# Kernel tuning notes

Hardware: AMD Instinct MI355X
Metric: run time of the kernel (lower is better)

## Reference

```python
import jax, jax.numpy as jnp
import numpy as np
import math

T, C = 8192, 1024

def setup_inputs() -> dict:
    key = jax.random.key(0)
    ks = jax.random.split(key, 10)
    s = 1.0 / math.sqrt(C)
    return {
        "x": jax.random.normal(ks[0], (T, C), dtype=jnp.float32),
        "Wq": jax.random.normal(ks[1], (C, C), dtype=jnp.float32) * s,
        "bq": jax.random.normal(ks[2], (C,), dtype=jnp.float32) * s,
        "Wk": jax.random.normal(ks[3], (C, C), dtype=jnp.float32) * s,
        "bk": jax.random.normal(ks[4], (C,), dtype=jnp.float32) * s,
        "Wv": jax.random.normal(ks[5], (C, C), dtype=jnp.float32) * s,
        "bv": jax.random.normal(ks[6], (C,), dtype=jnp.float32) * s,
        "Wp": jax.random.normal(ks[7], (C, C), dtype=jnp.float32) * s,
        "bp": jax.random.normal(ks[8], (C,), dtype=jnp.float32) * s,
    }

def reference(x, Wq, bq, Wk, bk, Wv, bv, Wp, bp):
    # Single-head causal self-attention over an unbatched (T, C) sequence.
    t, c = x.shape
    q = x @ Wq.T + bq          # (T, C)
    k = x @ Wk.T + bk          # (T, C)
    v = x @ Wv.T + bv          # (T, C)
    att = (q @ k.T) / math.sqrt(c)                      # (T, T)
    causal = jnp.tril(jnp.ones((t, t), dtype=bool))
    att = jnp.where(causal, att, -jnp.inf)
    att = jax.nn.softmax(att, axis=-1)
    y = att @ v                                         # (T, C)
    y = y @ Wp.T + bp
    return y
```

## Files before the change

### kernel.cpp

```cpp
#include <hip/hip_runtime.h>
#include <hip/hip_bf16.h>

typedef __bf16 bf16x8 __attribute__((ext_vector_type(8)));
typedef float f32x4 __attribute__((ext_vector_type(4)));

static constexpr int Tn = 8192;
static constexpr int Cn = 1024;

#define DEVI __device__ __forceinline__

DEVI float bf2f(ushort u) { union { uint i; float f; } c; c.i = ((uint)u) << 16; return c.f; }
DEVI ushort f2bf(float f) {
  uint x = __builtin_bit_cast(uint, f);
  x += 0x7fffu + ((x >> 16) & 1u);
  return (ushort)(x >> 16);
}

typedef const __attribute__((address_space(1))) void glb_v;
typedef __attribute__((address_space(3))) void lds_v;

__global__ __launch_bounds__(256) void cast_all(
    const float* __restrict__ x, const float* __restrict__ wq, const float* __restrict__ wk,
    const float* __restrict__ wv, const float* __restrict__ wp,
    ushort* __restrict__ xb, ushort* __restrict__ wqb, ushort* __restrict__ wkb,
    ushort* __restrict__ wvb, ushort* __restrict__ wpb)
{
  const long long NX = (long long)Tn * Cn;
  const long long NW = (long long)Cn * Cn;
  long long i = ((long long)blockIdx.x * 256 + threadIdx.x) * 4;
  const float* src; ushort* dst; long long off;
  if (i < NX) { src = x; dst = xb; off = i; }
  else {
    long long r = i - NX; int seg = (int)(r >> 20); off = r & (NW - 1);
    src = seg == 0 ? wq : seg == 1 ? wk : seg == 2 ? wv : wp;
    dst = seg == 0 ? wqb : seg == 1 ? wkb : seg == 2 ? wvb : wpb;
  }
  float4 v = *reinterpret_cast<const float4*>(src + off);
  ushort4 o; o.x = f2bf(v.x); o.y = f2bf(v.y); o.z = f2bf(v.z); o.w = f2bf(v.w);
  *reinterpret_cast<ushort4*>(dst + off) = o;
}

template<bool OUT_BF16, bool HAS_BIAS, bool CAUSAL_SKIP, bool KLIMIT>
__global__ __launch_bounds__(256, 2)
void gemm_bt(const ushort* __restrict__ A, const ushort* __restrict__ Bt,
             const float* __restrict__ bias, void* __restrict__ outp,
             int M, int N, int K, float scale)
{
  const int bx = blockIdx.x;
  int by = KLIMIT ? (gridDim.y - 1 - blockIdx.y) : blockIdx.y;
  if (CAUSAL_SKIP && by < bx) return;

  __shared__ ushort Als[128 * 64];
  __shared__ ushort Bls[128 * 64];

  const int tid = threadIdx.x;
  const int lane = tid & 63;
  const int wid = tid >> 6;
  const int wr = (wid >> 1) * 64, wc = (wid & 1) * 64;
  const int ln15 = lane & 15, lhi = lane >> 4;
  const int aRow0 = by * 128, bCol0 = bx * 128;

  int Keff = K;
  if (KLIMIT) { int lim = (by + 1) * 128; Keff = lim < K ? lim : K; }
  const int nkt = Keff >> 6;

  f32x4 acc[4][4] = {};

  for (int kt = 0; kt < nkt; ++kt) {
    const int k0 = kt << 6;
#pragma unroll
    for (int i = 0; i < 4; ++i) {
      int c = tid + i * 256;
      int row = c >> 3, kc = c & 7;
      int kcs = kc ^ (row & 7);
      const ushort* ga = A + (size_t)(aRow0 + row) * (size_t)K + (k0 + kcs * 8);
      const ushort* gb = Bt + (size_t)(bCol0 + row) * (size_t)K + (k0 + kcs * 8);
      __builtin_amdgcn_global_load_lds((glb_v*)ga, (lds_v*)(&Als[c * 8]), 16, 0, 0);
      __builtin_amdgcn_global_load_lds((glb_v*)gb, (lds_v*)(&Bls[c * 8]), 16, 0, 0);
    }
    __syncthreads();
#pragma unroll
    for (int kk = 0; kk < 2; ++kk) {
      bf16x8 af[4], bfr[4];
#pragma unroll
      for (int mi = 0; mi < 4; ++mi) {
        int r = wr + mi * 16 + ln15;
        int kc = kk * 4 + lhi;
        int slot = r * 8 + (kc ^ (r & 7));
        af[mi] = *reinterpret_cast<const bf16x8*>(&Als[slot * 8]);
      }
#pragma unroll
      for (int ni = 0; ni < 4; ++ni) {
        int r = wc + ni * 16 + ln15;
        int kc = kk * 4 + lhi;
        int slot = r * 8 + (kc ^ (r & 7));
        bfr[ni] = *reinterpret_cast<const bf16x8*>(&Bls[slot * 8]);
      }
#pragma unroll
      for (int mi = 0; mi < 4; ++mi)
#pragma unroll
        for (int ni = 0; ni < 4; ++ni)
          acc[mi][ni] = __builtin_amdgcn_mfma_f32_16x16x32_bf16(af[mi], bfr[ni], acc[mi][ni], 0, 0, 0);
    }
    __syncthreads();
  }

#pragma unroll
  for (int ni = 0; ni < 4; ++ni) {
    int col = bCol0 + wc + ni * 16 + ln15;
    float bv = HAS_BIAS ? bias[col] : 0.f;
#pragma unroll
    for (int mi = 0; mi < 4; ++mi) {
      f32x4 v = acc[mi][ni];
      int r0 = aRow0 + wr + mi * 16 + lhi * 4;
#pragma unroll
      for (int j = 0; j < 4; ++j) {
        float val = v[j] * scale + bv;
        if (OUT_BF16) ((ushort*)outp)[(size_t)(r0 + j) * N + col] = f2bf(val);
        else          ((float*)outp)[(size_t)(r0 + j) * N + col] = val;
      }
    }
  }
}

__global__ __launch_bounds__(256) void transpose64(const ushort* __restrict__ in,
                                                   ushort* __restrict__ out, int R, int Cin)
{
  __shared__ ushort tile[64][65];
  const int c0 = blockIdx.x * 64, r0 = blockIdx.y * 64;
  const int t = threadIdx.x;
#pragma unroll
  for (int i = t; i < 512; i += 256) {
    int r = i >> 3, kc = i & 7;
    uint4 v = *reinterpret_cast<const uint4*>(in + (size_t)(r0 + r) * Cin + c0 + kc * 8);
    const ushort* u = reinterpret_cast<const ushort*>(&v);
#pragma unroll
    for (int j = 0; j < 8; ++j) tile[r][kc * 8 + j] = u[j];
  }
  __syncthreads();
#pragma unroll
  for (int i = t; i < 512; i += 256) {
    int c = i >> 3, rc = i & 7;
    union { uint4 v; ushort u[8]; } pk;
#pragma unroll
    for (int j = 0; j < 8; ++j) pk.u[j] = tile[rc * 8 + j][c];
    *reinterpret_cast<uint4*>(out + (size_t)(c0 + c) * R + r0 + rc * 8) = pk.v;
  }
}

__global__ __launch_bounds__(256) void softmax_causal(ushort* __restrict__ S, int Td)
{
  const int t = blockIdx.x;
  const int tid = threadIdx.x;
  ushort* row = S + (size_t)t * Td;
  const int L = t + 1;
  const int Lv = L & ~7;

  float sum = 0.f;
  for (int j = tid * 8; j < Lv; j += 2048) {
    uint4 v = *reinterpret_cast<const uint4*>(row + j);
    const ushort* u = reinterpret_cast<const ushort*>(&v);
#pragma unroll
    for (int e = 0; e < 8; ++e) sum += __expf(bf2f(u[e]));
  }
  for (int j = Lv + tid; j < L; j += 256) sum += __expf(bf2f(row[j]));

#pragma unroll
  for (int off = 32; off; off >>= 1) sum += __shfl_down(sum, off);
  __shared__ float red[4];
  if ((tid & 63) == 0) red[tid >> 6] = sum;
  __syncthreads();
  const float inv = 1.f / (red[0] + red[1] + red[2] + red[3]);

  for (int j = tid * 8; j < Lv; j += 2048) {
    uint4 v = *reinterpret_cast<const uint4*>(row + j);
    union { uint4 v; ushort u[8]; } pk;
    const ushort* u = reinterpret_cast<const ushort*>(&v);
#pragma unroll
    for (int e = 0; e < 8; ++e) pk.u[e] = f2bf(__expf(bf2f(u[e])) * inv);
    *reinterpret_cast<uint4*>(row + j) = pk.v;
  }
  for (int j = Lv + tid; j < L; j += 256) row[j] = f2bf(__expf(bf2f(row[j])) * inv);

  const int Za = (L + 7) & ~7;
  for (int j = L + tid; j < Za; j += 256) row[j] = 0;
  uint4 z; z.x = z.y = z.z = z.w = 0u;
  for (int j = Za + tid * 8; j < Td; j += 2048) *reinterpret_cast<uint4*>(row + j) = z;
}

extern "C" void kernel_launch(void* const* d_in, const int* in_sizes, int n_in,
                              void* d_out, int out_size, void* d_ws, size_t ws_size,
                              hipStream_t stream)
{
  (void)in_sizes; (void)n_in; (void)out_size; (void)ws_size;
  const float* x  = (const float*)d_in[0];
  const float* Wq = (const float*)d_in[1];
  const float* bq = (const float*)d_in[2];
  const float* Wk = (const float*)d_in[3];
  const float* bk = (const float*)d_in[4];
  const float* Wv = (const float*)d_in[5];
  const float* bv = (const float*)d_in[6];
  const float* Wp = (const float*)d_in[7];
  const float* bp = (const float*)d_in[8];

  char* w = (char*)d_ws;
  const size_t TC = (size_t)Tn * Cn * 2, CC = (size_t)Cn * Cn * 2;
  ushort* xb  = (ushort*)w; w += TC;
  ushort* wqb = (ushort*)w; w += CC;
  ushort* wkb = (ushort*)w; w += CC;
  ushort* wvb = (ushort*)w; w += CC;
  ushort* wpb = (ushort*)w; w += CC;
  ushort* Qb  = (ushort*)w; w += TC;
  ushort* Kb  = (ushort*)w; w += TC;
  ushort* Vb  = (ushort*)w; w += TC;
  ushort* Vt  = (ushort*)w; w += TC;
  ushort* Yb  = (ushort*)w; w += TC;
  ushort* S   = (ushort*)w; w += (size_t)Tn * Tn * 2;

  cast_all<<<12288, 256, 0, stream>>>(x, Wq, Wk, Wv, Wp, xb, wqb, wkb, wvb, wpb);

  dim3 gp(Cn / 128, Tn / 128);
  gemm_bt<true, true, false, false><<<gp, 256, 0, stream>>>(xb, wqb, bq, Qb, Tn, Cn, Cn, 1.0f);
  gemm_bt<true, true, false, false><<<gp, 256, 0, stream>>>(xb, wkb, bk, Kb, Tn, Cn, Cn, 1.0f);
  gemm_bt<true, true, false, false><<<gp, 256, 0, stream>>>(xb, wvb, bv, Vb, Tn, Cn, Cn, 1.0f);

  transpose64<<<dim3(Cn / 64, Tn / 64), 256, 0, stream>>>(Vb, Vt, Tn, Cn);

  gemm_bt<true, false, true, false><<<dim3(Tn / 128, Tn / 128), 256, 0, stream>>>(
      Qb, Kb, nullptr, S, Tn, Tn, Cn, 0.03125f);

  softmax_causal<<<Tn, 256, 0, stream>>>(S, Tn);

  gemm_bt<true, false, false, true><<<gp, 256, 0, stream>>>(S, Vt, nullptr, Yb, Tn, Cn, Tn, 1.0f);

  gemm_bt<false, true, false, false><<<gp, 256, 0, stream>>>(Yb, wpb, bp, d_out, Tn, Cn, Cn, 1.0f);
}
```

Before: 370.8 us.

## Fuse QKV projections into one GEMM and launch only lower-triangle score tiles

Concatenates the Q, K and V weights and biases during the cast step so a single GEMM launch over 24 column tiles writes Q, K and V through a split epilogue. The QK^T launch now covers only the 2080 lower-triangle tiles, mapped from a linear block id with a sqrt-based decode and a row-interleaving swizzle, instead of launching a full grid and exiting early. The launch_bounds occupancy hint of two blocks per SM is dropped. These changes cut launch count and idle blocks and give better wave fill, at the cost of extra index arithmetic and possibly different register allocation.

```diff
diff --git a/kernel.cpp b/kernel.cpp
--- a/kernel.cpp
+++ b/kernel.cpp
@@ -22,59 +22,77 @@
 __global__ __launch_bounds__(256) void cast_all(
     const float* __restrict__ x, const float* __restrict__ wq, const float* __restrict__ wk,
     const float* __restrict__ wv, const float* __restrict__ wp,
-    ushort* __restrict__ xb, ushort* __restrict__ wqb, ushort* __restrict__ wkb,
-    ushort* __restrict__ wvb, ushort* __restrict__ wpb)
+    const float* __restrict__ bq, const float* __restrict__ bk, const float* __restrict__ bv,
+    ushort* __restrict__ xb, ushort* __restrict__ wqkv, ushort* __restrict__ wpb,
+    float* __restrict__ bqkv)
 {
   const long long NX = (long long)Tn * Cn;
   const long long NW = (long long)Cn * Cn;
+  if (blockIdx.x >= 12288) {
+    int id = ((blockIdx.x - 12288) * 256 + threadIdx.x) * 4;
+#pragma unroll
+    for (int e = 0; e < 4; ++e) {
+      int j = id + e;
+      if (j < 3 * Cn) bqkv[j] = j < Cn ? bq[j] : (j < 2 * Cn ? bk[j - Cn] : bv[j - 2 * Cn]);
+    }
+    return;
+  }
   long long i = ((long long)blockIdx.x * 256 + threadIdx.x) * 4;
   const float* src; ushort* dst; long long off;
   if (i < NX) { src = x; dst = xb; off = i; }
   else {
     long long r = i - NX; int seg = (int)(r >> 20); off = r & (NW - 1);
-    src = seg == 0 ? wq : seg == 1 ? wk : seg == 2 ? wv : wp;
-    dst = seg == 0 ? wqb : seg == 1 ? wkb : seg == 2 ? wvb : wpb;
+    if (seg < 3) { src = seg == 0 ? wq : seg == 1 ? wk : wv; dst = wqkv + (size_t)seg * NW; }
+    else         { src = wp; dst = wpb; }
   }
   float4 v = *reinterpret_cast<const float4*>(src + off);
   ushort4 o; o.x = f2bf(v.x); o.y = f2bf(v.y); o.z = f2bf(v.z); o.w = f2bf(v.w);
   *reinterpret_cast<ushort4*>(dst + off) = o;
 }
 
-template<bool OUT_BF16, bool HAS_BIAS, bool CAUSAL_SKIP, bool KLIMIT>
-__global__ __launch_bounds__(256, 2)
-void gemm_bt(const ushort* __restrict__ A, const ushort* __restrict__ Bt,
-             const float* __restrict__ bias, void* __restrict__ outp,
-             int M, int N, int K, float scale)
-{
-  const int bx = blockIdx.x;
-  int by = KLIMIT ? (gridDim.y - 1 - blockIdx.y) : blockIdx.y;
-  if (CAUSAL_SKIP && by < bx) return;
-
-  __shared__ ushort Als[128 * 64];
-  __shared__ ushort Bls[128 * 64];
+template<bool OUT_BF16, bool HAS_BIAS, bool TRI, bool PVMODE, bool SPLIT3>
+__global__ __launch_bounds__(256)
+void gemm_tlp(const ushort* __restrict__ A, const ushort* __restrict__ Bt,
+              const float* __restrict__ bias, void* __restrict__ outp,
+              int K, int lda, int ldb, int ldc, float scale)
+{
+  __shared__ __align__(16) ushort Als[128 * 64];
+  __shared__ __align__(16) ushort Bls[128 * 64];
 
   const int tid = threadIdx.x;
-  const int lane = tid & 63;
-  const int wid = tid >> 6;
+  const int lane = tid & 63, wid = tid >> 6;
   const int wr = (wid >> 1) * 64, wc = (wid & 1) * 64;
   const int ln15 = lane & 15, lhi = lane >> 4;
-  const int aRow0 = by * 128, bCol0 = bx * 128;
-
-  int Keff = K;
-  if (KLIMIT) { int lim = (by + 1) * 128; Keff = lim < K ? lim : K; }
-  const int nkt = Keff >> 6;
+
+  int bx, by;
+  if (TRI) {
+    int id = blockIdx.x;
+    int sw = (id & 7) * ((int)gridDim.x >> 3) + (id >> 3);
+    float ff = __builtin_sqrtf(8.f * (float)sw + 1.f);
+    by = (int)((ff - 1.f) * 0.5f);
+    while ((by + 1) * (by + 2) / 2 <= sw) ++by;
+    while (by * (by + 1) / 2 > sw) --by;
+    bx = sw - by * (by + 1) / 2;
+  } else {
+    bx = blockIdx.x;
+    by = PVMODE ? ((int)gridDim.y - 1 - (int)blockIdx.y) : (int)blockIdx.y;
+  }
+
+  const int rowA0 = by * 128, col0 = bx * 128;
+  int NT = K >> 6;
+  if (PVMODE) { int kl = (by + 1) * 128; if (kl < K) NT = kl >> 6; }
 
   f32x4 acc[4][4] = {};
 
-  for (int kt = 0; kt < nkt; ++kt) {
+  for (int kt = 0; kt < NT; ++kt) {
     const int k0 = kt << 6;
 #pragma unroll
     for (int i = 0; i < 4; ++i) {
       int c = tid + i * 256;
       int row = c >> 3, kc = c & 7;
       int kcs = kc ^ (row & 7);
-      const ushort* ga = A + (size_t)(aRow0 + row) * (size_t)K + (k0 + kcs * 8);
-      const ushort* gb = Bt + (size_t)(bCol0 + row) * (size_t)K + (k0 + kcs * 8);
+      const ushort* ga = A + (size_t)(rowA0 + row) * (size_t)lda + (k0 + kcs * 8);
+      const ushort* gb = Bt + (size_t)(col0 + row) * (size_t)ldb + (k0 + kcs * 8);
       __builtin_amdgcn_global_load_lds((glb_v*)ga, (lds_v*)(&Als[c * 8]), 16, 0, 0);
       __builtin_amdgcn_global_load_lds((glb_v*)gb, (lds_v*)(&Bls[c * 8]), 16, 0, 0);
     }
@@ -86,15 +104,13 @@
       for (int mi = 0; mi < 4; ++mi) {
         int r = wr + mi * 16 + ln15;
         int kc = kk * 4 + lhi;
-        int slot = r * 8 + (kc ^ (r & 7));
-        af[mi] = *reinterpret_cast<const bf16x8*>(&Als[slot * 8]);
+        af[mi] = *reinterpret_cast<const bf16x8*>(&Als[(r * 8 + (kc ^ (r & 7))) * 8]);
       }
 #pragma unroll
       for (int ni = 0; ni < 4; ++ni) {
         int r = wc + ni * 16 + ln15;
         int kc = kk * 4 + lhi;
-        int slot = r * 8 + (kc ^ (r & 7));
-        bfr[ni] = *reinterpret_cast<const bf16x8*>(&Bls[slot * 8]);
+        bfr[ni] = *reinterpret_cast<const bf16x8*>(&Bls[(r * 8 + (kc ^ (r & 7))) * 8]);
       }
 #pragma unroll
       for (int mi = 0; mi < 4; ++mi)
@@ -107,24 +123,28 @@
 
 #pragma unroll
   for (int ni = 0; ni < 4; ++ni) {
-    int col = bCol0 + wc + ni * 16 + ln15;
-    float bv = HAS_BIAS ? bias[col] : 0.f;
+    int colg = col0 + wc + ni * 16 + ln15;
+    float bv = HAS_BIAS ? bias[colg] : 0.f;
+    int col = colg;
+    size_t segoff = 0;
+    if (SPLIT3) { int seg = colg >> 10; col = colg & 1023; segoff = (size_t)seg * (size_t)Tn * Cn; }
 #pragma unroll
     for (int mi = 0; mi < 4; ++mi) {
       f32x4 v = acc[mi][ni];
-      int r0 = aRow0 + wr + mi * 16 + lhi * 4;
+      int r0 = rowA0 + wr + mi * 16 + lhi * 4;
 #pragma unroll
       for (int j = 0; j < 4; ++j) {
         float val = v[j] * scale + bv;
-        if (OUT_BF16) ((ushort*)outp)[(size_t)(r0 + j) * N + col] = f2bf(val);
-        else          ((float*)outp)[(size_t)(r0 + j) * N + col] = val;
+        if (OUT_BF16) ((ushort*)outp)[segoff + (size_t)(r0 + j) * (size_t)ldc + col] = f2bf(val);
+        else          ((float*)outp)[segoff + (size_t)(r0 + j) * (size_t)ldc + col] = val;
       }
     }
   }
 }
 
 __global__ __launch_bounds__(256) void transpose64(const ushort* __restrict__ in,
-                                                   ushort* __restrict__ out, int R, int Cin)
+                                                   ushort* __restrict__ out,
+                                                   int ldin, int ldout)
 {
   __shared__ ushort tile[64][65];
   const int c0 = blockIdx.x * 64, r0 = blockIdx.y * 64;
@@ -132,7 +152,7 @@
 #pragma unroll
   for (int i = t; i < 512; i += 256) {
     int r = i >> 3, kc = i & 7;
-    uint4 v = *reinterpret_cast<const uint4*>(in + (size_t)(r0 + r) * Cin + c0 + kc * 8);
+    uint4 v = *reinterpret_cast<const uint4*>(in + (size_t)(r0 + r) * ldin + c0 + kc * 8);
     const ushort* u = reinterpret_cast<const ushort*>(&v);
 #pragma unroll
     for (int j = 0; j < 8; ++j) tile[r][kc * 8 + j] = u[j];
@@ -144,7 +164,7 @@
     union { uint4 v; ushort u[8]; } pk;
 #pragma unroll
     for (int j = 0; j < 8; ++j) pk.u[j] = tile[rc * 8 + j][c];
-    *reinterpret_cast<uint4*>(out + (size_t)(c0 + c) * R + r0 + rc * 8) = pk.v;
+    *reinterpret_cast<uint4*>(out + (size_t)(c0 + c) * ldout + r0 + rc * 8) = pk.v;
   }
 }
 
@@ -205,33 +225,32 @@
 
   char* w = (char*)d_ws;
   const size_t TC = (size_t)Tn * Cn * 2, CC = (size_t)Cn * Cn * 2;
-  ushort* xb  = (ushort*)w; w += TC;
-  ushort* wqb = (ushort*)w; w += CC;
-  ushort* wkb = (ushort*)w; w += CC;
-  ushort* wvb = (ushort*)w; w += CC;
-  ushort* wpb = (ushort*)w; w += CC;
-  ushort* Qb  = (ushort*)w; w += TC;
-  ushort* Kb  = (ushort*)w; w += TC;
-  ushort* Vb  = (ushort*)w; w += TC;
-  ushort* Vt  = (ushort*)w; w += TC;
-  ushort* Yb  = (ushort*)w; w += TC;
-  ushort* S   = (ushort*)w; w += (size_t)Tn * Tn * 2;
-
-  cast_all<<<12288, 256, 0, stream>>>(x, Wq, Wk, Wv, Wp, xb, wqb, wkb, wvb, wpb);
-
-  dim3 gp(Cn / 128, Tn / 128);
-  gemm_bt<true, true, false, false><<<gp, 256, 0, stream>>>(xb, wqb, bq, Qb, Tn, Cn, Cn, 1.0f);
-  gemm_bt<true, true, false, false><<<gp, 256, 0, stream>>>(xb, wkb, bk, Kb, Tn, Cn, Cn, 1.0f);
-  gemm_bt<true, true, false, false><<<gp, 256, 0, stream>>>(xb, wvb, bv, Vb, Tn, Cn, Cn, 1.0f);
-
-  transpose64<<<dim3(Cn / 64, Tn / 64), 256, 0, stream>>>(Vb, Vt, Tn, Cn);
-
-  gemm_bt<true, false, true, false><<<dim3(Tn / 128, Tn / 128), 256, 0, stream>>>(
-      Qb, Kb, nullptr, S, Tn, Tn, Cn, 0.03125f);
+  ushort* xb   = (ushort*)w; w += TC;
+  ushort* Wqkv = (ushort*)w; w += 3 * CC;
+  ushort* wpb  = (ushort*)w; w += CC;
+  float*  bqkv = (float*)w;  w += 3 * Cn * 4 + 4096;
+  ushort* Qb   = (ushort*)w; w += TC;
+  ushort* Kb   = (ushort*)w; w += TC;
+  ushort* Vb   = (ushort*)w; w += TC;
+  ushort* Vt   = (ushort*)w; w += TC;
+  ushort* Yb   = (ushort*)w; w += TC;
+  ushort* S    = (ushort*)w; w += (size_t)Tn * Tn * 2;
+
+  cast_all<<<12291, 256, 0, stream>>>(x, Wq, Wk, Wv, Wp, bq, bk, bv, xb, Wqkv, wpb, bqkv);
+
+  gemm_tlp<true, true, false, false, true><<<dim3(24, 64), 256, 0, stream>>>(
+      xb, Wqkv, bqkv, Qb, Cn, Cn, Cn, Cn, 1.0f);
+
+  transpose64<<<dim3(Cn / 64, Tn / 64), 256, 0, stream>>>(Vb, Vt, Cn, Tn);
+
+  gemm_tlp<true, false, true, false, false><<<dim3(2080, 1), 256, 0, stream>>>(
+      Qb, Kb, nullptr, S, Cn, Cn, Cn, Tn, 0.03125f);
 
   softmax_causal<<<Tn, 256, 0, stream>>>(S, Tn);
 
-  gemm_bt<true, false, false, true><<<gp, 256, 0, stream>>>(S, Vt, nullptr, Yb, Tn, Cn, Tn, 1.0f);
-
-  gemm_bt<false, true, false, false><<<gp, 256, 0, stream>>>(Yb, wpb, bp, d_out, Tn, Cn, Cn, 1.0f);
-}
+  gemm_tlp<true, false, false, true, false><<<dim3(8, 64), 256, 0, stream>>>(
+      S, Vt, nullptr, Yb, Tn, Tn, Tn, Cn, 1.0f);
+
+  gemm_tlp<false, true, false, false, false><<<dim3(8, 64), 256, 0, stream>>>(
+      Yb, wpb, bp, d_out, Cn, Cn, Cn, Cn, 1.0f);
+}
```

After: 399.6 us. +7.8%, slower.
